# Kernel optimization log

Hardware: AMD Instinct MI355X
Metric: run time of the kernel (lower is better)

Reference implementation:

```python
import jax, jax.numpy as jnp
import numpy as np

B, C_LEN, Q_LEN, D = 8, 2048, 512, 1024


def setup_inputs() -> dict:
    key = jax.random.key(0)
    ks = jax.random.split(key, 10)
    scale = 1.0 / np.sqrt(D)
    return {
        "c": jax.random.normal(ks[0], (B, C_LEN, D), dtype=jnp.float32),
        "q": jax.random.normal(ks[1], (B, Q_LEN, D), dtype=jnp.float32),
        "w_cq": jax.random.normal(ks[2], (D,), dtype=jnp.float32) * scale,
        "b_cq": jax.random.normal(ks[3], (), dtype=jnp.float32) * scale,
        "w_c": jax.random.normal(ks[4], (D,), dtype=jnp.float32) * scale,
        "b_c": jax.random.normal(ks[5], (), dtype=jnp.float32) * scale,
        "w_q": jax.random.normal(ks[6], (D,), dtype=jnp.float32) * scale,
        "b_q": jax.random.normal(ks[7], (), dtype=jnp.float32) * scale,
        "W_l": jax.random.normal(ks[8], (D, 4 * D), dtype=jnp.float32) * (1.0 / np.sqrt(4 * D)),
        "b_l": jax.random.normal(ks[9], (D,), dtype=jnp.float32) * (1.0 / np.sqrt(4 * D)),
    }


def reference(c, q, w_cq, b_cq, w_c, b_c, w_q, b_q, W_l, b_l):
    # trilinear term: the original loops over q positions computing
    # att_weight_cq(c * q_i); since that Linear is rank-1, this is one einsum.
    cq = jnp.einsum('bcd,bqd,d->bcq', c, q, w_cq) + b_cq        # [B, C, Q]
    s = (c @ w_c + b_c)[:, :, None] + (q @ w_q + b_q)[:, None, :] + cq
    a = jax.nn.softmax(s, axis=2)                               # c2q attention
    c2q_att = jnp.einsum('bcq,bqd->bcd', a, q)                  # [B, C, D]
    b_att = jax.nn.softmax(jnp.max(s, axis=2), axis=1)          # [B, C]
    q2c_att = jnp.einsum('bc,bcd->bd', b_att, c)[:, None, :]    # [B, 1, D]
    x = jnp.concatenate([c, c2q_att, c * c2q_att, c * q2c_att], axis=-1)
    z = x @ W_l.T + b_l                                         # [B, C, D]
    return z
```

## Files before the change

### kernel.cpp

```cpp
#include <hip/hip_runtime.h>

typedef unsigned short u16;
typedef __attribute__((ext_vector_type(4))) float floatx4;
typedef __attribute__((ext_vector_type(4))) unsigned short u16x4;
typedef __attribute__((ext_vector_type(8))) short short8;
typedef __attribute__((ext_vector_type(8))) __bf16 bf16x8;

#define B_SZ 8
#define C_LEN 2048
#define Q_LEN 512
#define D_DIM 1024
#define K4 (4 * D_DIM)

static __device__ __forceinline__ u16 f2bf(float f) {
    union { float f; unsigned int u; } v; v.f = f;
    unsigned int r = v.u + 0x7FFFu + ((v.u >> 16) & 1u);
    return (u16)(r >> 16);
}
static __device__ __forceinline__ float bf2f(u16 h) {
    union { unsigned int u; float f; } v; v.u = ((unsigned int)h) << 16;
    return v.f;
}

static __device__ __forceinline__ void async16(const void* g, void* l) {
    __builtin_amdgcn_global_load_lds(
        (const __attribute__((address_space(1))) unsigned int*)g,
        (__attribute__((address_space(3))) unsigned int*)(unsigned int)(unsigned long long)l,
        16, 0, 0);
}

__global__ __launch_bounds__(256) void prep_kernel(
    const float* __restrict__ c, const float* __restrict__ q,
    const float* __restrict__ w_cq, const float* __restrict__ w_c, const float* __restrict__ w_q,
    u16* __restrict__ cbf, u16* __restrict__ qwbf, u16* __restrict__ qT,
    float* __restrict__ rowterm, float* __restrict__ colterm, float* __restrict__ q2c) {
    int blk = blockIdx.x;
    int tid = threadIdx.x;
    if (blk < 4096) {
        int row = blk * 4 + (tid >> 6);
        int lane = tid & 63;
        const float* src = c + (size_t)row * D_DIM;
        u16* dst = cbf + (size_t)row * D_DIM;
        float s = 0.f;
        #pragma unroll
        for (int j = 0; j < 4; ++j) {
            int idx = j * 256 + lane * 4;
            floatx4 a = *(const floatx4*)(src + idx);
            floatx4 w = *(const floatx4*)(w_c + idx);
            s += a[0]*w[0] + a[1]*w[1] + a[2]*w[2] + a[3]*w[3];
            u16x4 o;
            #pragma unroll
            for (int e = 0; e < 4; ++e) o[e] = f2bf(a[e]);
            *(u16x4*)(dst + idx) = o;
        }
        for (int off = 32; off; off >>= 1) s += __shfl_down(s, off);
        if (lane == 0) rowterm[row] = s;
    } else if (blk < 5120) {
        int row = (blk - 4096) * 4 + (tid >> 6);
        int lane = tid & 63;
        const float* src = q + (size_t)row * D_DIM;
        u16* dst = qwbf + (size_t)row * D_DIM;
        float s = 0.f;
        #pragma unroll
        for (int j = 0; j < 4; ++j) {
            int idx = j * 256 + lane * 4;
            floatx4 a  = *(const floatx4*)(src + idx);
            floatx4 wc = *(const floatx4*)(w_cq + idx);
            floatx4 wq = *(const floatx4*)(w_q + idx);
            s += a[0]*wq[0] + a[1]*wq[1] + a[2]*wq[2] + a[3]*wq[3];
            u16x4 o;
            #pragma unroll
            for (int e = 0; e < 4; ++e) o[e] = f2bf(a[e] * wc[e]);
            *(u16x4*)(dst + idx) = o;
        }
        for (int off = 32; off; off >>= 1) s += __shfl_down(s, off);
        if (lane == 0) colterm[row] = s;
    } else if (blk < 9216) {
        __shared__ float tile[32][33];
        int t = blk - 5120;
        int q0 = (t & 15) * 32;
        int d0 = ((t >> 4) & 31) * 32;
        int b = t >> 9;
        int tx = tid & 31, ty = tid >> 5;
        const float* qb = q + (size_t)b * Q_LEN * D_DIM;
        #pragma unroll
        for (int j = 0; j < 4; ++j) {
            int row = ty + j * 8;
            tile[row][tx] = qb[(size_t)(q0 + row) * D_DIM + d0 + tx];
        }
        __syncthreads();
        u16* qTb = qT + (size_t)b * D_DIM * Q_LEN;
        #pragma unroll
        for (int j = 0; j < 4; ++j) {
            int row = ty + j * 8;
            qTb[(size_t)(d0 + row) * Q_LEN + q0 + tx] = f2bf(tile[tx][row]);
        }
    } else {
        int i = (blk - 9216) * 256 + tid;
        q2c[i] = 0.0f;
    }
}

__global__ __launch_bounds__(256) void wmerge_all(const float* __restrict__ W, const float* __restrict__ q2c,
                                                  u16* __restrict__ Wm, u16* __restrict__ Wbf) {
    int n = blockIdx.x;
    int k = threadIdx.x * 4;
    const float* wr = W + (size_t)n * K4;
    floatx4 w1 = *(const floatx4*)(wr + k);
    floatx4 w4 = *(const floatx4*)(wr + 3072 + k);
    #pragma unroll
    for (int p = 0; p < 2; ++p) {
        int kk = p * 1024 + k;
        floatx4 v = *(const floatx4*)(wr + 1024 + kk);
        u16x4 o;
        #pragma unroll
        for (int e = 0; e < 4; ++e) o[e] = f2bf(v[e]);
        *(u16x4*)(Wbf + (size_t)n * 2048 + kk) = o;
    }
    #pragma unroll
    for (int b = 0; b < 8; ++b) {
        floatx4 g = *(const floatx4*)(q2c + (size_t)b * D_DIM + k);
        u16x4 o;
        #pragma unroll
        for (int e = 0; e < 4; ++e) o[e] = f2bf(w1[e] + w4[e] * g[e]);
        *(u16x4*)(Wm + (size_t)b * 1048576 + (size_t)n * 1024 + k) = o;
    }
}

template<int MODE>
__global__ __launch_bounds__(256) void gemm_async(
    const u16* __restrict__ A0, const u16* __restrict__ A1, const u16* __restrict__ A2,
    const u16* __restrict__ B0, const u16* __restrict__ B1,
    float* __restrict__ of, u16* __restrict__ ob, const float* __restrict__ bias) {
    constexpr int NSEC = (MODE == 2) ? 3 : 1;
    constexpr int KSEC = (MODE == 1) ? 512 : 1024;
    constexpr int LDO  = (MODE == 0) ? 512 : 1024;
    constexpr int NTILES = (MODE == 0) ? 4 : 8;
    __shared__ u16 As[128 * 64];
    __shared__ u16 Bs[128 * 64];
    const int tid  = threadIdx.x;
    const int lane = tid & 63;
    const int wave = tid >> 6;
    const int lin  = blockIdx.x;
    const int b    = lin & 7;
    const int rem  = lin >> 3;
    const int n0   = (rem % NTILES) * 128;
    const int m0   = (rem / NTILES) * 128;

    const u16* Aarr[NSEC];
    const u16* Barr[NSEC];
    int lda_[NSEC], ldb_[NSEC];
    if constexpr (MODE == 0) {
        Aarr[0] = A0 + (size_t)b * C_LEN * D_DIM; lda_[0] = 1024;
        Barr[0] = B0 + (size_t)b * Q_LEN * D_DIM; ldb_[0] = 1024;
    } else if constexpr (MODE == 1) {
        Aarr[0] = A0 + (size_t)b * C_LEN * Q_LEN; lda_[0] = 512;
        Barr[0] = B0 + (size_t)b * D_DIM * Q_LEN; ldb_[0] = 512;
    } else {
        Aarr[0] = A0 + (size_t)b * C_LEN * D_DIM;  lda_[0] = 1024;
        Barr[0] = B0 + (size_t)b * D_DIM * D_DIM;  ldb_[0] = 1024;
        Aarr[1] = A1 + (size_t)b * C_LEN * 2048;        lda_[1] = 2048;
        Barr[1] = B1;                                   ldb_[1] = 2048;
        Aarr[2] = A1 + (size_t)b * C_LEN * 2048 + 1024; lda_[2] = 2048;
        Barr[2] = B1 + 1024;                            ldb_[2] = 2048;
    }

    const int srow = lane >> 3;
    const int ssc  = ((lane & 7) ^ srow) * 8;

    floatx4 acc[4][4];
    #pragma unroll
    for (int i = 0; i < 4; ++i)
        #pragma unroll
        for (int j = 0; j < 4; ++j)
            acc[i][j] = (floatx4)(0.0f);

    const int wrow = (wave >> 1) * 64;
    const int wcol = (wave & 1) * 64;
    const int quad = lane >> 4;
    const int lrow = lane & 15;
    const int sw7  = lane & 7;

    #pragma unroll
    for (int sec = 0; sec < NSEC; ++sec) {
        const u16* __restrict__ Ab = Aarr[sec];
        const u16* __restrict__ Bb = Barr[sec];
        const int LA = lda_[sec];
        const int LB = ldb_[sec];
        for (int k0 = 0; k0 < KSEC; k0 += 64) {
            #pragma unroll
            for (int cc = 0; cc < 4; ++cc) {
                int ch = wave * 4 + cc;
                int rr = ch * 8 + srow;
                async16(Ab + (size_t)(m0 + rr) * LA + k0 + ssc, &As[ch * 512]);
            }
            #pragma unroll
            for (int cc = 0; cc < 4; ++cc) {
                int ch = wave * 4 + cc;
                int rr = ch * 8 + srow;
                async16(Bb + (size_t)(n0 + rr) * LB + k0 + ssc, &Bs[ch * 512]);
            }
            __syncthreads();
            #pragma unroll
            for (int h = 0; h < 2; ++h) {
                const int pc = ((h * 4 + quad) ^ sw7) * 8;
                bf16x8 af[4], bfr[4];
                #pragma unroll
                for (int i = 0; i < 4; ++i)
                    af[i] = __builtin_bit_cast(bf16x8, *(const short8*)&As[(wrow + i*16 + lrow) * 64 + pc]);
                #pragma unroll
                for (int j = 0; j < 4; ++j)
                    bfr[j] = __builtin_bit_cast(bf16x8, *(const short8*)&Bs[(wcol + j*16 + lrow) * 64 + pc]);
                #pragma unroll
                for (int i = 0; i < 4; ++i)
                    #pragma unroll
                    for (int j = 0; j < 4; ++j)
                        acc[i][j] = __builtin_amdgcn_mfma_f32_16x16x32_bf16(af[i], bfr[j], acc[i][j], 0, 0, 0);
            }
            __syncthreads();
        }
    }

    float* ofb = nullptr; u16* ccb = nullptr; const u16* cbr = nullptr;
    if (MODE == 0)      ofb = of + (size_t)b * C_LEN * Q_LEN;
    else if (MODE == 1) { ccb = ob + (size_t)b * C_LEN * 2048; cbr = A1 + (size_t)b * C_LEN * D_DIM; }
    else                ofb = of + (size_t)b * C_LEN * D_DIM;
    #pragma unroll
    for (int i = 0; i < 4; ++i) {
        #pragma unroll
        for (int j = 0; j < 4; ++j) {
            #pragma unroll
            for (int e = 0; e < 4; ++e) {
                int gm = m0 + wrow + i * 16 + quad * 4 + e;
                int gn = n0 + wcol + j * 16 + lrow;
                float v = acc[i][j][e];
                if (MODE == 0)      ofb[(size_t)gm * LDO + gn] = v;
                else if (MODE == 1) {
                    u16 p = f2bf(v);
                    float cv = bf2f(cbr[(size_t)gm * 1024 + gn]);
                    ccb[(size_t)gm * 2048 + gn]        = p;
                    ccb[(size_t)gm * 2048 + 1024 + gn] = f2bf(cv * bf2f(p));
                }
                else                ofb[(size_t)gm * LDO + gn] = v + bias[gn];
            }
        }
    }
}

#define PIN() __builtin_amdgcn_sched_barrier(0)
#define BAR8() do { PIN(); __builtin_amdgcn_s_barrier(); PIN(); } while (0)
#define VMW(N) do { asm volatile("s_waitcnt vmcnt(" #N ")" ::: "memory"); } while (0)

#define LDA4(DST, MQ, KH, CUR) do { \
    const u16* un_ = lds_ + (CUR) * 32768 + (KH) * 8192; \
    _Pragma("unroll") \
    for (int i_ = 0; i_ < 4; ++i_) \
      (DST)[i_] = __builtin_bit_cast(bf16x8, \
          *(const short8*)(un_ + (wm * 128 + (MQ) * 64 + i_ * 16 + lrow) * 32 + pcs)); \
  } while (0)

#define LDB4(DST, KH, CUR) do { \
    const u16* un_ = lds_ + (CUR) * 32768 + 16384 + (KH) * 8192; \
    _Pragma("unroll") \
    for (int i_ = 0; i_ < 4; ++i_) \
      (DST)[i_] = __builtin_bit_cast(bf16x8, \
          *(const short8*)(un_ + (wn * 64 + i_ * 16 + lrow) * 32 + pcs)); \
  } while (0)

#define MFMA16(MQ4, A_, B_) do { \
    __builtin_amdgcn_s_setprio(1); \
    _Pragma("unroll") \
    for (int i_ = 0; i_ < 4; ++i_) { \
      _Pragma("unroll") \
      for (int j_ = 0; j_ < 4; ++j_) \
        acc[(MQ4) + i_][j_] = __builtin_amdgcn_mfma_f32_16x16x32_bf16( \
            (A_)[i_], (B_)[j_], acc[(MQ4) + i_][j_], 0, 0, 0); \
    } \
    __builtin_amdgcn_s_setprio(0); \
  } while (0)

__global__ __launch_bounds__(512, 2) void gemm2_8ph(
    const u16* __restrict__ cbf, const u16* __restrict__ CC,
    const u16* __restrict__ Wm, const u16* __restrict__ Wbf,
    float* __restrict__ of, const float* __restrict__ bias) {
    __shared__ __align__(16) u16 lds_[65536];
    const int tid  = threadIdx.x;
    const int lane = tid & 63;
    const int wave = tid >> 6;
    const int lin  = blockIdx.x;
    const int b    = lin & 7;
    const int rem  = lin >> 3;
    const int n0   = (rem & 3) * 256;
    const int m0   = (rem >> 2) * 256;
    const int wm   = wave >> 2;
    const int wn   = wave & 3;
    const int quad = lane >> 4;
    const int lrow = lane & 15;
    const int pcs  = (quad ^ (lrow & 3)) * 8;

    const u16* Acb  = cbf + (size_t)b * (C_LEN * D_DIM);
    const u16* Acc0 = CC  + (size_t)b * (C_LEN * 2048);
    const u16* Acc1 = Acc0 + 1024;
    const u16* Bwm  = Wm  + (size_t)b * (D_DIM * D_DIM);

    auto STAGE = [&](int tt, int ab, int kh) {
        const int sec = tt >> 4;
        const int kl  = (tt & 15) * 64 + kh * 32;
        const u16* base;
        int r0;
        if (ab == 0) { base = (sec == 0) ? Acb : (sec == 1) ? Acc0 : Acc1; r0 = m0; }
        else         { base = (sec == 0) ? Bwm : (sec == 1) ? Wbf  : Wbf + 1024; r0 = n0; }
        const int ld = (sec == 0) ? 1024 : 2048;
        u16* unit = lds_ + (tt & 1) * 32768 + ab * 16384 + kh * 8192;
        #pragma unroll
        for (int l = 0; l < 2; ++l) {
            const int li  = l * 512 + tid;
            const int row = li >> 2;
            const int sc  = (li & 3) ^ (row & 3);
            async16(base + (size_t)(r0 + row) * ld + kl + sc * 8,
                    unit + (l * 512 + (tid & ~63)) * 8);
        }
    };

    floatx4 acc[8][4];
    #pragma unroll
    for (int i = 0; i < 8; ++i)
        #pragma unroll
        for (int j = 0; j < 4; ++j) acc[i][j] = (floatx4)(0.0f);

    STAGE(0, 1, 0); PIN(); STAGE(0, 0, 0); PIN(); STAGE(0, 1, 1); PIN(); STAGE(0, 0, 1); PIN();
    STAGE(1, 1, 0); PIN(); STAGE(1, 0, 0); PIN(); STAGE(1, 1, 1); PIN();
    VMW(10);
    BAR8();

    bf16x8 af[4], bf[4];
    for (int tt = 0; tt < 48; ++tt) {
        const int cur = tt & 1;
        if (tt + 1 < 48) STAGE(tt + 1, 0, 1);
        LDA4(af, 0, 0, cur);
        LDB4(bf, 0, cur);
        BAR8();
        MFMA16(0, af, bf);
        BAR8();
        if (tt + 2 < 48) STAGE(tt + 2, 1, 0);
        LDA4(af, 1, 0, cur);
        BAR8();
        MFMA16(4, af, bf);
        if (tt < 46) VMW(10); else VMW(0);
        BAR8();
        if (tt + 2 < 48) STAGE(tt + 2, 0, 0);
        LDA4(af, 0, 1, cur);
        LDB4(bf, 1, cur);
        BAR8();
        MFMA16(0, af, bf);
        BAR8();
        if (tt + 2 < 48) STAGE(tt + 2, 1, 1);
        LDA4(af, 1, 1, cur);
        BAR8();
        MFMA16(4, af, bf);
        if (tt < 46) VMW(10); else VMW(0);
        BAR8();
    }

    float bs[4];
    #pragma unroll
    for (int j = 0; j < 4; ++j) bs[j] = bias[n0 + wn * 64 + j * 16 + lrow];
    float* ofb = of + (size_t)b * (C_LEN * D_DIM);
    #pragma unroll
    for (int i = 0; i < 8; ++i) {
        #pragma unroll
        for (int j = 0; j < 4; ++j) {
            #pragma unroll
            for (int e = 0; e < 4; ++e) {
                const int gm = m0 + wm * 128 + i * 16 + quad * 4 + e;
                const int gn = n0 + wn * 64 + j * 16 + lrow;
                ofb[(size_t)gm * D_DIM + gn] = acc[i][j][e] + bs[j];
            }
        }
    }
}

__global__ void softmax_kernel(const float* __restrict__ S, const float* __restrict__ colterm,
                               u16* __restrict__ P, float* __restrict__ mbuf) {
    int row = blockIdx.x * 4 + (threadIdx.x >> 6);
    int lane = threadIdx.x & 63;
    int b = row >> 11;
    const float* sp = S + (size_t)row * Q_LEN;
    const float* cp = colterm + (size_t)b * Q_LEN;
    float v[8];
    float m = -1e30f;
    #pragma unroll
    for (int j = 0; j < 8; ++j) {
        int idx = j * 64 + lane;
        v[j] = sp[idx] + cp[idx];
        m = fmaxf(m, v[j]);
    }
    for (int off = 32; off; off >>= 1) m = fmaxf(m, __shfl_xor(m, off));
    float s = 0.f;
    #pragma unroll
    for (int j = 0; j < 8; ++j) { v[j] = __expf(v[j] - m); s += v[j]; }
    for (int off = 32; off; off >>= 1) s += __shfl_xor(s, off);
    float inv = 1.0f / s;
    u16* pp = P + (size_t)row * Q_LEN;
    #pragma unroll
    for (int j = 0; j < 8; ++j) pp[j * 64 + lane] = f2bf(v[j] * inv);
    if (lane == 0) mbuf[row] = m;
}

__global__ __launch_bounds__(256) void batt_kernel(const float* __restrict__ mbuf,
                                                   const float* __restrict__ rowterm,
                                                   float* __restrict__ batt) {
    __shared__ float red[8];
    int b = blockIdx.x;
    int tid = threadIdx.x;
    const float* mb = mbuf + (size_t)b * C_LEN;
    const float* rt = rowterm + (size_t)b * C_LEN;
    float v[8];
    float m = -1e30f;
    #pragma unroll
    for (int j = 0; j < 8; ++j) { int idx = j * 256 + tid; v[j] = mb[idx] + rt[idx]; m = fmaxf(m, v[j]); }
    for (int off = 32; off; off >>= 1) m = fmaxf(m, __shfl_xor(m, off));
    int wave = tid >> 6, lane = tid & 63;
    if (lane == 0) red[wave] = m;
    __syncthreads();
    m = fmaxf(fmaxf(red[0], red[1]), fmaxf(red[2], red[3]));
    float s = 0.f;
    #pragma unroll
    for (int j = 0; j < 8; ++j) { v[j] = __expf(v[j] - m); s += v[j]; }
    for (int off = 32; off; off >>= 1) s += __shfl_xor(s, off);
    if (lane == 0) red[4 + wave] = s;
    __syncthreads();
    s = red[4] + red[5] + red[6] + red[7];
    float inv = 1.0f / s;
    float* bb = batt + (size_t)b * C_LEN;
    #pragma unroll
    for (int j = 0; j < 8; ++j) bb[j * 256 + tid] = v[j] * inv;
}

__global__ __launch_bounds__(256) void q2c_kernel(const float* __restrict__ batt,
                                                  const u16* __restrict__ cbf,
                                                  float* __restrict__ q2c) {
    int d  = blockIdx.x * 256 + threadIdx.x;
    int b  = blockIdx.y;
    int c0 = blockIdx.z * 256;
    const u16* cb = cbf + ((size_t)b * C_LEN + c0) * D_DIM + d;
    const float* bb = batt + (size_t)b * C_LEN + c0;
    float s = 0.f;
    #pragma unroll 4
    for (int i = 0; i < 256; ++i) s += bb[i] * bf2f(cb[(size_t)i * D_DIM]);
    atomicAdd(&q2c[(size_t)b * D_DIM + d], s);
}

extern "C" void kernel_launch(void* const* d_in, const int* in_sizes, int n_in,
                              void* d_out, int out_size, void* d_ws, size_t ws_size,
                              hipStream_t stream) {
    const float* c   = (const float*)d_in[0];
    const float* q   = (const float*)d_in[1];
    const float* wcq = (const float*)d_in[2];
    const float* w_c = (const float*)d_in[4];
    const float* w_q = (const float*)d_in[6];
    const float* W_l = (const float*)d_in[8];
    const float* b_l = (const float*)d_in[9];
    float* out = (float*)d_out;

    char* ws = (char*)d_ws;
    u16*   cbf     = (u16*)ws;
    float* S       = (float*)(ws + 33554432);
    u16*   CC      = (u16*)(ws + 33554432);
    u16*   qwbf    = (u16*)(ws + 67108864);
    u16*   P       = (u16*)(ws + 100663296);
    u16*   Wm      = (u16*)(ws + 100663296);
    u16*   qT      = (u16*)(ws + 117440512);
    u16*   Wbf     = (u16*)(ws + 117440512);
    float* rowterm = (float*)(ws + 125829120);
    float* colterm = (float*)(ws + 125894656);
    float* mbuf    = (float*)(ws + 125911040);
    float* batt    = (float*)(ws + 125976576);
    float* q2c     = (float*)(ws + 126042112);

    prep_kernel<<<dim3(9248), dim3(256), 0, stream>>>(c, q, wcq, w_c, w_q,
                                                      cbf, qwbf, qT, rowterm, colterm, q2c);
    gemm_async<0><<<dim3(512), dim3(256), 0, stream>>>(cbf, nullptr, nullptr, qwbf, nullptr, S, nullptr, nullptr);
    softmax_kernel<<<dim3(4096), dim3(256), 0, stream>>>(S, colterm, P, mbuf);
    batt_kernel<<<dim3(8), dim3(256), 0, stream>>>(mbuf, rowterm, batt);
    q2c_kernel<<<dim3(4, 8, 8), dim3(256), 0, stream>>>(batt, cbf, q2c);
    gemm_async<1><<<dim3(1024), dim3(256), 0, stream>>>(P, cbf, nullptr, qT, nullptr, nullptr, CC, nullptr);
    wmerge_all<<<dim3(1024), dim3(256), 0, stream>>>(W_l, q2c, Wm, Wbf);
    gemm2_8ph<<<dim3(256), dim3(512), 0, stream>>>(cbf, CC, Wm, Wbf, out, b_l);
}
```

Before: 358.0 us.

## Stage full 64-wide K tiles per operand with 8-way LDS swizzle

Changes the LDS tile layout in the final GEMM from two 32-column K-halves to one 64-column row with an XOR swizzle over 8 chunks. Each operand tile is now loaded in a single staging call of four async copies instead of two calls of two. The per-iteration schedule shrinks from four stage points with vmcnt(10) waits to two stage points with vmcnt(4) waits. The intent is to make global loads wider and more contiguous, cut bank conflicts and simplify the prefetch pipeline, at the risk of less finely interleaved loads and changed overlap timing.

After: 348.9 us. 1.03x faster.

```diff
diff --git a/kernel.cpp b/kernel.cpp
--- a/kernel.cpp
+++ b/kernel.cpp
@@ -252,19 +252,19 @@
 #define VMW(N) do { asm volatile("s_waitcnt vmcnt(" #N ")" ::: "memory"); } while (0)
 
 #define LDA4(DST, MQ, KH, CUR) do { \
-    const u16* un_ = lds_ + (CUR) * 32768 + (KH) * 8192; \
+    const u16* un_ = lds_ + (CUR) * 32768; \
     _Pragma("unroll") \
     for (int i_ = 0; i_ < 4; ++i_) \
       (DST)[i_] = __builtin_bit_cast(bf16x8, \
-          *(const short8*)(un_ + (wm * 128 + (MQ) * 64 + i_ * 16 + lrow) * 32 + pcs)); \
+          *(const short8*)(un_ + (wm * 128 + (MQ) * 64 + i_ * 16 + lrow) * 64 + pca[KH])); \
   } while (0)
 
 #define LDB4(DST, KH, CUR) do { \
-    const u16* un_ = lds_ + (CUR) * 32768 + 16384 + (KH) * 8192; \
+    const u16* un_ = lds_ + (CUR) * 32768 + 16384; \
     _Pragma("unroll") \
     for (int i_ = 0; i_ < 4; ++i_) \
       (DST)[i_] = __builtin_bit_cast(bf16x8, \
-          *(const short8*)(un_ + (wn * 64 + i_ * 16 + lrow) * 32 + pcs)); \
+          *(const short8*)(un_ + (wn * 64 + i_ * 16 + lrow) * 64 + pca[KH])); \
   } while (0)
 
 #define MFMA16(MQ4, A_, B_) do { \
@@ -296,29 +296,30 @@
     const int wn   = wave & 3;
     const int quad = lane >> 4;
     const int lrow = lane & 15;
-    const int pcs  = (quad ^ (lrow & 3)) * 8;
+    const int lr7  = lane & 7;
+    const int pca[2] = { ((0 + quad) ^ lr7) * 8, ((4 + quad) ^ lr7) * 8 };
 
     const u16* Acb  = cbf + (size_t)b * (C_LEN * D_DIM);
     const u16* Acc0 = CC  + (size_t)b * (C_LEN * 2048);
     const u16* Acc1 = Acc0 + 1024;
     const u16* Bwm  = Wm  + (size_t)b * (D_DIM * D_DIM);
 
-    auto STAGE = [&](int tt, int ab, int kh) {
+    auto STAGE = [&](int tt, int ab) {
         const int sec = tt >> 4;
-        const int kl  = (tt & 15) * 64 + kh * 32;
+        const int kl  = (tt & 15) * 64;
         const u16* base;
         int r0;
         if (ab == 0) { base = (sec == 0) ? Acb : (sec == 1) ? Acc0 : Acc1; r0 = m0; }
         else         { base = (sec == 0) ? Bwm : (sec == 1) ? Wbf  : Wbf + 1024; r0 = n0; }
         const int ld = (sec == 0) ? 1024 : 2048;
-        u16* unit = lds_ + (tt & 1) * 32768 + ab * 16384 + kh * 8192;
-        #pragma unroll
-        for (int l = 0; l < 2; ++l) {
+        u16* unit = lds_ + (tt & 1) * 32768 + ab * 16384;
+        #pragma unroll
+        for (int l = 0; l < 4; ++l) {
             const int li  = l * 512 + tid;
-            const int row = li >> 2;
-            const int sc  = (li & 3) ^ (row & 3);
+            const int row = li >> 3;
+            const int sc  = (li & 7) ^ (row & 7);
             async16(base + (size_t)(r0 + row) * ld + kl + sc * 8,
-                    unit + (l * 512 + (tid & ~63)) * 8);
+                    unit + (size_t)(l * 512 + (tid & ~63)) * 8);
         }
     };
 
@@ -328,37 +329,33 @@
         #pragma unroll
         for (int j = 0; j < 4; ++j) acc[i][j] = (floatx4)(0.0f);
 
-    STAGE(0, 1, 0); PIN(); STAGE(0, 0, 0); PIN(); STAGE(0, 1, 1); PIN(); STAGE(0, 0, 1); PIN();
-    STAGE(1, 1, 0); PIN(); STAGE(1, 0, 0); PIN(); STAGE(1, 1, 1); PIN();
-    VMW(10);
+    STAGE(0, 0); PIN(); STAGE(0, 1); PIN(); STAGE(1, 1); PIN();
+    VMW(4);
     BAR8();
 
     bf16x8 af[4], bf[4];
     for (int tt = 0; tt < 48; ++tt) {
         const int cur = tt & 1;
-        if (tt + 1 < 48) STAGE(tt + 1, 0, 1);
+        if (tt + 1 < 48) STAGE(tt + 1, 0);
         LDA4(af, 0, 0, cur);
         LDB4(bf, 0, cur);
         BAR8();
         MFMA16(0, af, bf);
         BAR8();
-        if (tt + 2 < 48) STAGE(tt + 2, 1, 0);
         LDA4(af, 1, 0, cur);
         BAR8();
         MFMA16(4, af, bf);
-        if (tt < 46) VMW(10); else VMW(0);
-        BAR8();
-        if (tt + 2 < 48) STAGE(tt + 2, 0, 0);
+        BAR8();
         LDA4(af, 0, 1, cur);
         LDB4(bf, 1, cur);
         BAR8();
         MFMA16(0, af, bf);
         BAR8();
-        if (tt + 2 < 48) STAGE(tt + 2, 1, 1);
+        if (tt + 2 < 48) STAGE(tt + 2, 1);
         LDA4(af, 1, 1, cur);
         BAR8();
         MFMA16(4, af, bf);
-        if (tt < 46) VMW(10); else VMW(0);
+        if (tt < 46) { VMW(4); } else { VMW(0); }
         BAR8();
     }
 
```
